# Performance work log

Hardware: AMD Instinct MI355X
Metric: run time of the kernel (lower is better)

Reference implementation:

```python
import jax, jax.numpy as jnp
import numpy as np


def setup_inputs() -> dict:
    key = jax.random.key(0)
    k1, k2, k3 = jax.random.split(key, 3)
    B, Lc, Lq, D = 16, 1024, 1024, 256
    context_features = jax.random.normal(k1, (B, Lc, D), dtype=jnp.float32)
    question_features = jax.random.normal(k2, (B, Lq, D), dtype=jnp.float32)
    # nn.Linear(3D, 1, bias=False) weight, stored transposed as [3D, 1]
    weight = jax.random.normal(k3, (3 * D, 1), dtype=jnp.float32) * (1.0 / np.sqrt(3 * D))
    return {"context_features": context_features, "question_features": question_features, "weight": weight}


def reference(context_features, question_features, weight):
    # Trilinear similarity: sim[b,i,j] = [c_i ; q_j ; c_i*q_j] @ w
    # Decompose w = [wc ; wq ; wm] (each D) to avoid the O(B*Lc*Lq*3D) tensor:
    # sim = c@wc + q@wq + (c*wm) @ q^T   -- exact same math as the concat+Linear.
    D = context_features.shape[-1]
    w = weight[:, 0]
    wc, wq, wm = w[:D], w[D:2 * D], w[2 * D:]
    sim = (
        jnp.einsum('bcd,d->bc', context_features, wc)[:, :, None]
        + jnp.einsum('bqd,d->bq', question_features, wq)[:, None, :]
        + jnp.einsum('bcd,bqd->bcq', context_features * wm, question_features)
    )  # [B, Lc, Lq]
    weight_c2q = jax.nn.softmax(sim, axis=-1)                      # [B, Lc, Lq]
    c2q = jnp.einsum('bcq,bqd->bcd', weight_c2q, question_features)
    weight_q2c = jax.nn.softmax(jnp.max(sim, axis=2), axis=-1)     # [B, Lc]
    q2c = jnp.einsum('bc,bcd->bd', weight_q2c, context_features)   # [B, D]
    q2c = jnp.broadcast_to(q2c[:, None, :], c2q.shape)             # repeat over Lc
    return (c2q, q2c)
```

## Files before the change

### kernel.cpp

```cpp
#include <hip/hip_runtime.h>
#include <math.h>

#define BB 16
#define LC 1024
#define LQ 1024
#define DD 256

#define CTB 64
#define QTB 64
#define QT_S 72

typedef __attribute__((ext_vector_type(4))) float f32x4;
typedef __attribute__((ext_vector_type(8))) short bf16x8;
typedef __attribute__((ext_vector_type(4))) short bf16x4;

__device__ inline short f2bf(float f) {
    union { float f; unsigned u; } v; v.f = f;
    unsigned r = v.u + 0x7FFFu + ((v.u >> 16) & 1u);
    return (short)(r >> 16);
}


__global__ __launch_bounds__(256) void k_prep(const float* __restrict__ qst,
                                              const float* __restrict__ w,
                                              short* __restrict__ Qbf,
                                              short* __restrict__ Qtbf,
                                              float* __restrict__ qterm) {
    __shared__ short Qt_lds[DD][QT_S];
    int t = threadIdx.x;
    int qt = blockIdx.x;
    int b  = blockIdx.y;
    int wv4 = t >> 6;
    int l   = t & 63;
    int lx  = l & 15;
    int ls  = l >> 4;

    #pragma unroll
    for (int kq = 0; kq < 4; ++kq) {
        int ql = 16 * wv4 + 4 * kq + ls;
        float qpart = 0.f;
        #pragma unroll
        for (int jd = 0; jd < 4; ++jd) {
            int d0 = 64 * jd + 4 * lx;
            float4 x = *(const float4*)(qst + ((size_t)(b * LQ + qt * QTB + ql)) * DD + d0);
            float4 wq = *(const float4*)(w + DD + d0);
            qpart += x.x * wq.x + x.y * wq.y + x.z * wq.z + x.w * wq.w;
            bf16x4 o;
            o[0] = f2bf(x.x); o[1] = f2bf(x.y); o[2] = f2bf(x.z); o[3] = f2bf(x.w);
            *(bf16x4*)(Qbf + ((size_t)(b * LQ + qt * QTB + ql)) * DD + d0) = o;
            float X[4] = {x.x, x.y, x.z, x.w};
            float P1[4], X1[4], P2[4], X2[4];
            #pragma unroll
            for (int e = 0; e < 4; ++e) P1[e] = __shfl_xor(X[e ^ 1], 16);
            #pragma unroll
            for (int e = 0; e < 4; ++e) X1[e] = ((ls & 1) == (e & 1)) ? X[e] : P1[e];
            #pragma unroll
            for (int e = 0; e < 4; ++e) P2[e] = __shfl_xor(X1[e ^ 2], 32);
            #pragma unroll
            for (int e = 0; e < 4; ++e) X2[e] = ((ls & 2) == (e & 2)) ? X1[e] : P2[e];
            int dl = 64 * jd + 4 * lx + ls;
            bf16x4 ot;
            ot[0] = f2bf(X2[0]); ot[1] = f2bf(X2[1]); ot[2] = f2bf(X2[2]); ot[3] = f2bf(X2[3]);
            *(bf16x4*)&Qt_lds[dl][16 * wv4 + 4 * kq] = ot;
        }
        qpart += __shfl_xor(qpart, 1);
        qpart += __shfl_xor(qpart, 2);
        qpart += __shfl_xor(qpart, 4);
        qpart += __shfl_xor(qpart, 8);
        if (lx == 0) qterm[b * LQ + qt * QTB + ql] = qpart;
    }
    __syncthreads();
    #pragma unroll
    for (int rep = 0; rep < 8; ++rep) {
        int d   = rep * 32 + (t >> 3);
        int qch = t & 7;
        bf16x8 v = *(const bf16x8*)&Qt_lds[d][8 * qch];
        *(bf16x8*)(Qtbf + ((size_t)(b * DD + d)) * LQ + qt * QTB + 8 * qch) = v;
    }
}

__global__ __launch_bounds__(512) void k_main(const float* __restrict__ ctx,
                                              const short* __restrict__ Qbf,
                                              const short* __restrict__ Qtbf,
                                              const float* __restrict__ wght,
                                              const float* __restrict__ ws,
                                              float* __restrict__ out,
                                              float* __restrict__ rowmax_out) {
    __shared__ short CMp[4 * 8 * 512];
    __shared__ short sPp[2][4 * 2 * 512];
    __shared__ float scaleS[2][CTB];
    __shared__ float mS[2][CTB], lS[2][CTB];
    __shared__ float ctermS[2][CTB];
    __shared__ float mergebuf[4 * 64 * 20];

    const int t  = threadIdx.x;
    const int wv = t >> 6;
    const int g  = wv >> 2;
    const int w4 = wv & 3;
    const int l  = t & 63;
    const int lx = l & 15;
    const int ls = l >> 4;
    const int bid = blockIdx.x;
    const int b  = bid & 15;
    const int c0 = (bid >> 4) * CTB;

    const float* qterm = ws;

    {
        const int kh = g * 4;
        int cl = 16 * w4 + lx;
        float cpart = 0.f;
        #pragma unroll
        for (int kq = 0; kq < 4; ++kq) {
            int kk = kh + kq;
            int d0 = 32 * kk + 8 * ls;
            const float4 x0 = *(const float4*)(ctx + ((size_t)(b * LC + c0 + cl)) * DD + d0);
            const float4 x1 = *(const float4*)(ctx + ((size_t)(b * LC + c0 + cl)) * DD + d0 + 4);
            const float4 w0 = *(const float4*)(wght + 2 * DD + d0);
            const float4 w1 = *(const float4*)(wght + 2 * DD + d0 + 4);
            const float4 c0v = *(const float4*)(wght + d0);
            const float4 c1v = *(const float4*)(wght + d0 + 4);
            cpart += x0.x * c0v.x + x0.y * c0v.y + x0.z * c0v.z + x0.w * c0v.w
                   + x1.x * c1v.x + x1.y * c1v.y + x1.z * c1v.z + x1.w * c1v.w;
            bf16x8 o;
            o[0] = f2bf(x0.x * w0.x); o[1] = f2bf(x0.y * w0.y);
            o[2] = f2bf(x0.z * w0.z); o[3] = f2bf(x0.w * w0.w);
            o[4] = f2bf(x1.x * w1.x); o[5] = f2bf(x1.y * w1.y);
            o[6] = f2bf(x1.z * w1.z); o[7] = f2bf(x1.w * w1.w);
            *(bf16x8*)&CMp[(w4 * 8 + kk) * 512 + l * 8] = o;
        }
        cpart += __shfl_xor(cpart, 16);
        cpart += __shfl_xor(cpart, 32);
        if (ls == 0) ctermS[g][cl] = cpart;
    }

    float mrun[4], lrun[4];
    f32x4 oacc[4][4];
    #pragma unroll
    for (int r = 0; r < 4; ++r) { mrun[r] = -1e30f; lrun[r] = 0.f; }
    #pragma unroll
    for (int cf = 0; cf < 4; ++cf)
        #pragma unroll
        for (int df = 0; df < 4; ++df)
            oacc[cf][df] = (f32x4){0.f, 0.f, 0.f, 0.f};

    __syncthreads();

    for (int it = 0; it < 8; ++it) {
        const int qtile = 2 * it + g;
        const size_t qbase = (size_t)b * LQ + qtile * QTB;

        f32x4 sacc[4];
        #pragma unroll
        for (int f = 0; f < 4; ++f) sacc[f] = (f32x4){0.f, 0.f, 0.f, 0.f};
        bf16x8 bA[4][4], bB[4][4];
        #pragma unroll
        for (int kk = 0; kk < 4; ++kk)
            #pragma unroll
            for (int f = 0; f < 4; ++f)
                bA[kk][f] = *(const bf16x8*)(Qbf + (qbase + 16 * f + lx) * DD + 32 * kk + 8 * ls);
        bf16x8 acur = *(const bf16x8*)&CMp[(w4 * 8 + 0) * 512 + l * 8];
        #pragma unroll
        for (int kk = 0; kk < 4; ++kk) {
            bf16x8 anext = *(const bf16x8*)&CMp[(w4 * 8 + kk + 1) * 512 + l * 8];
            #pragma unroll
            for (int f = 0; f < 4; ++f)
                bB[kk][f] = *(const bf16x8*)(Qbf + (qbase + 16 * f + lx) * DD + 32 * (kk + 4) + 8 * ls);
            #pragma unroll
            for (int f = 0; f < 4; ++f)
                sacc[f] = __builtin_amdgcn_mfma_f32_16x16x32_bf16(acur, bA[kk][f], sacc[f], 0, 0, 0);
            acur = anext;
        }
        #pragma unroll
        for (int kk = 4; kk < 8; ++kk) {
            bf16x8 anext = (kk < 7) ? *(const bf16x8*)&CMp[(w4 * 8 + kk + 1) * 512 + l * 8] : acur;
            #pragma unroll
            for (int f = 0; f < 4; ++f)
                sacc[f] = __builtin_amdgcn_mfma_f32_16x16x32_bf16(acur, bB[kk - 4][f], sacc[f], 0, 0, 0);
            acur = anext;
        }

        bf16x8 qtb[2][4];
        #pragma unroll
        for (int kk = 0; kk < 2; ++kk)
            #pragma unroll
            for (int df = 0; df < 4; ++df)
                qtb[kk][df] = *(const bf16x8*)(Qtbf + ((size_t)(b * DD + 64 * w4 + 16 * df + lx)) * LQ
                                               + qtile * QTB + 32 * kk + 8 * ls);

        float qv[4];
        #pragma unroll
        for (int f = 0; f < 4; ++f) qv[f] = qterm[qbase + 16 * f + lx];
        #pragma unroll
        for (int f = 0; f < 4; ++f) {
            #pragma unroll
            for (int r = 0; r < 4; ++r) sacc[f][r] += qv[f];
        }
        float scl[4];
        #pragma unroll
        for (int r = 0; r < 4; ++r) {
            float v = fmaxf(fmaxf(sacc[0][r], sacc[1][r]), fmaxf(sacc[2][r], sacc[3][r]));
            v = fmaxf(v, __shfl_xor(v, 1));
            v = fmaxf(v, __shfl_xor(v, 2));
            v = fmaxf(v, __shfl_xor(v, 4));
            v = fmaxf(v, __shfl_xor(v, 8));
            float mn = fmaxf(mrun[r], v);
            scl[r] = __expf(mrun[r] - mn);
            mrun[r] = mn;
            lrun[r] *= scl[r];
        }
        float p[4][4];
        float rs[4] = {0.f, 0.f, 0.f, 0.f};
        #pragma unroll
        for (int f = 0; f < 4; ++f)
            #pragma unroll
            for (int r = 0; r < 4; ++r) {
                p[f][r] = __expf(sacc[f][r] - mrun[r]);
                rs[r] += p[f][r];
            }
        #pragma unroll
        for (int r = 0; r < 4; ++r) {
            float v = rs[r];
            v += __shfl_xor(v, 1);
            v += __shfl_xor(v, 2);
            v += __shfl_xor(v, 4);
            v += __shfl_xor(v, 8);
            lrun[r] += v;
        }
        #pragma unroll
        for (int f = 0; f < 4; ++f) {
            #pragma unroll
            for (int r = 0; r < 4; ++r) {
                int cl = 16 * w4 + 4 * ls + r;
                int ql = 16 * f + lx;
                int idx = ((cl >> 4) * 2 + (ql >> 5)) * 512 + ((cl & 15) + 16 * ((ql >> 3) & 3)) * 8 + (ql & 7);
                sPp[g][idx] = f2bf(p[f][r]);
            }
        }
        if (lx == 0) {
            #pragma unroll
            for (int r = 0; r < 4; ++r) scaleS[g][16 * w4 + 4 * ls + r] = scl[r];
        }
        __syncthreads();

        #pragma unroll
        for (int cf = 0; cf < 4; ++cf) {
            #pragma unroll
            for (int r = 0; r < 4; ++r) {
                float s = scaleS[g][16 * cf + 4 * ls + r];
                #pragma unroll
                for (int df = 0; df < 4; ++df) oacc[cf][df][r] *= s;
            }
        }
        bf16x8 pa[2][4];
        #pragma unroll
        for (int kk = 0; kk < 2; ++kk)
            #pragma unroll
            for (int cf = 0; cf < 4; ++cf)
                pa[kk][cf] = *(const bf16x8*)&sPp[g][(cf * 2 + kk) * 512 + l * 8];
        #pragma unroll
        for (int kk = 0; kk < 2; ++kk)
            #pragma unroll
            for (int df = 0; df < 4; ++df)
                #pragma unroll
                for (int cf = 0; cf < 4; ++cf)
                    oacc[cf][df] = __builtin_amdgcn_mfma_f32_16x16x32_bf16(pa[kk][cf], qtb[kk][df], oacc[cf][df], 0, 0, 0);
        __syncthreads();
    }

    if (lx == 0) {
        #pragma unroll
        for (int r = 0; r < 4; ++r) {
            mS[g][16 * w4 + 4 * ls + r] = mrun[r];
            lS[g][16 * w4 + 4 * ls + r] = lrun[r];
        }
    }
    __syncthreads();

    float alpha[4][4], ltot[4][4], mtot[4][4];
    #pragma unroll
    for (int cf = 0; cf < 4; ++cf) {
        #pragma unroll
        for (int r = 0; r < 4; ++r) {
            int cl = 16 * cf + 4 * ls + r;
            float m0 = mS[0][cl], m1 = mS[1][cl];
            float mx = fmaxf(m0, m1);
            float a0 = __expf(m0 - mx), a1 = __expf(m1 - mx);
            mtot[cf][r] = mx;
            ltot[cf][r] = a0 * lS[0][cl] + a1 * lS[1][cl];
            alpha[cf][r] = (g == 0) ? a0 : a1;
        }
    }
    #pragma unroll
    for (int cf = 0; cf < 4; ++cf) {
        #pragma unroll
        for (int df = 0; df < 4; ++df)
            #pragma unroll
            for (int r = 0; r < 4; ++r)
                oacc[cf][df][r] *= alpha[cf][r];
    }
    #pragma unroll
    for (int cf = 0; cf < 4; ++cf) {
        if (g == 1) {
            #pragma unroll
            for (int df = 0; df < 4; ++df)
                *(f32x4*)&mergebuf[(w4 * 64 + l) * 20 + df * 4] = oacc[cf][df];
        }
        __syncthreads();
        if (g == 0) {
            #pragma unroll
            for (int df = 0; df < 4; ++df) {
                f32x4 v = *(const f32x4*)&mergebuf[(w4 * 64 + l) * 20 + df * 4];
                oacc[cf][df][0] += v[0]; oacc[cf][df][1] += v[1];
                oacc[cf][df][2] += v[2]; oacc[cf][df][3] += v[3];
            }
        }
        __syncthreads();
    }

    if (g == 0) {
        if (wv == 0 && lx == 0) {
            #pragma unroll
            for (int cf = 0; cf < 4; ++cf)
                #pragma unroll
                for (int r = 0; r < 4; ++r) {
                    int cl = 16 * cf + 4 * ls + r;
                    int c = b * LC + c0 + cl;
                    rowmax_out[c] = mtot[cf][r] + ctermS[0][cl] + ctermS[1][cl];
                }
        }
        #pragma unroll
        for (int cf = 0; cf < 4; ++cf) {
            #pragma unroll
            for (int r = 0; r < 4; ++r) {
                float inv = 1.0f / ltot[cf][r];
                size_t row = (size_t)(b * LC + c0 + 16 * cf + 4 * ls + r) * DD;
                #pragma unroll
                for (int df = 0; df < 4; ++df)
                    out[row + 64 * w4 + 16 * df + lx] = oacc[cf][df][r] * inv;
            }
        }
    }
}

__global__ __launch_bounds__(256) void k_q2c(const float* __restrict__ ctx,
                                             const float* __restrict__ rowmax,
                                             float* __restrict__ q2cvec) {
    __shared__ float sm[LC];
    __shared__ float red[256];
    int b = blockIdx.x;
    int chunk = blockIdx.y;
    int t = threadIdx.x;
    const float* rm = rowmax + b * LC;

    float lmax = -1e30f;
    #pragma unroll
    for (int k = 0; k < 4; ++k) {
        float v = rm[t + k * 256];
        sm[t + k * 256] = v;
        lmax = fmaxf(lmax, v);
    }
    red[t] = lmax;
    __syncthreads();
    for (int s = 128; s > 0; s >>= 1) {
        if (t < s) red[t] = fmaxf(red[t], red[t + s]);
        __syncthreads();
    }
    float gmax = red[0];
    __syncthreads();
    float lsum = 0.f;
    #pragma unroll
    for (int k = 0; k < 4; ++k) {
        int i = t + k * 256;
        float e = __expf(sm[i] - gmax);
        sm[i] = e;
        lsum += e;
    }
    red[t] = lsum;
    __syncthreads();
    for (int s = 128; s > 0; s >>= 1) {
        if (t < s) red[t] += red[t + s];
        __syncthreads();
    }
    float inv = 1.0f / red[0];

    int c0 = chunk * 32;
    float acc = 0.f;
    for (int c = c0; c < c0 + 32; ++c)
        acc += sm[c] * ctx[(size_t)(b * LC + c) * DD + t];
    atomicAdd(&q2cvec[b * DD + t], acc * inv);
}

__global__ __launch_bounds__(256) void k_bcast(const float* __restrict__ q2cvec,
                                               float* __restrict__ out2) {
    int g = blockIdx.x * 256 + threadIdx.x;
    int b  = g >> 16;
    int d4 = g & 63;
    ((float4*)out2)[g] = ((const float4*)q2cvec)[b * 64 + d4];
}

extern "C" void kernel_launch(void* const* d_in, const int* in_sizes, int n_in,
                              void* d_out, int out_size, void* d_ws, size_t ws_size,
                              hipStream_t stream) {
    const float* ctx = (const float*)d_in[0];
    const float* qst = (const float*)d_in[1];
    const float* w   = (const float*)d_in[2];
    float* out  = (float*)d_out;
    float* out2 = out + (size_t)BB * LC * DD;
    float* ws   = (float*)d_ws;

    float* qterm  = ws;
    float* rowmax = ws + 32768;
    float* q2cvec = ws + 49152;
    short* Qbf  = (short*)out2;
    short* Qtbf = Qbf + (size_t)BB * LQ * DD;

    hipMemsetAsync(q2cvec, 0, BB * DD * sizeof(float), stream);

    k_prep<<<dim3(LQ / QTB, BB), 256, 0, stream>>>(qst, w, Qbf, Qtbf, qterm);

    k_main<<<(LC / CTB) * BB, 512, 0, stream>>>(ctx, Qbf, Qtbf, w, ws, out, rowmax);

    k_q2c<<<dim3(BB, 32), 256, 0, stream>>>(ctx, rowmax, q2cvec);

    k_bcast<<<(BB * LC * DD / 4) / 256, 256, 0, stream>>>(q2cvec, out2);
}
```

Measured before the change: 185.9 us.

## Split query loop across four wave groups with 1024-thread blocks; fold memset into prep

The main kernel now runs 1024 threads per block, so four wave groups each handle a quarter of the query tiles instead of two groups handling half each. Their flash-style partial softmax states are then merged through a shared LDS pool that is reused for the P tiles and the merge buffer. The separate memset of the q2c accumulator is moved into the prep kernel to save a launch. This gives more parallelism per context tile and fewer serial iterations per wave. In exchange it adds three sequential merge rounds with barriers, and the larger register and LDS footprint per block may reduce occupancy.

```diff
diff --git a/kernel.cpp b/kernel.cpp
--- a/kernel.cpp
+++ b/kernel.cpp
@@ -25,7 +25,8 @@
                                               const float* __restrict__ w,
                                               short* __restrict__ Qbf,
                                               short* __restrict__ Qtbf,
-                                              float* __restrict__ qterm) {
+                                              float* __restrict__ qterm,
+                                              float* __restrict__ q2cvec) {
     __shared__ short Qt_lds[DD][QT_S];
     int t = threadIdx.x;
     int qt = blockIdx.x;
@@ -34,6 +35,8 @@
     int l   = t & 63;
     int lx  = l & 15;
     int ls  = l >> 4;
+
+    if (qt == 0) q2cvec[b * DD + t] = 0.f;
 
     #pragma unroll
     for (int kq = 0; kq < 4; ++kq) {
@@ -79,19 +82,20 @@
     }
 }
 
-__global__ __launch_bounds__(512) void k_main(const float* __restrict__ ctx,
-                                              const short* __restrict__ Qbf,
-                                              const short* __restrict__ Qtbf,
-                                              const float* __restrict__ wght,
-                                              const float* __restrict__ ws,
-                                              float* __restrict__ out,
-                                              float* __restrict__ rowmax_out) {
-    __shared__ short CMp[4 * 8 * 512];
-    __shared__ short sPp[2][4 * 2 * 512];
-    __shared__ float scaleS[2][CTB];
-    __shared__ float mS[2][CTB], lS[2][CTB];
+__global__ __launch_bounds__(1024) void k_main(const float* __restrict__ ctx,
+                                               const short* __restrict__ Qbf,
+                                               const short* __restrict__ Qtbf,
+                                               const float* __restrict__ wght,
+                                               const float* __restrict__ ws,
+                                               float* __restrict__ out,
+                                               float* __restrict__ rowmax_out) {
+    __shared__ __align__(16) char pool[32768 + 256 * 68 * 4];
+    short* CMp = (short*)pool;
+    short* sPp = (short*)(pool + 32768);
+    float* mergebuf = (float*)(pool + 32768);
+    __shared__ float scaleS[4][CTB];
+    __shared__ float mS[4][CTB], lS[4][CTB];
     __shared__ float ctermS[2][CTB];
-    __shared__ float mergebuf[4 * 64 * 20];
 
     const int t  = threadIdx.x;
     const int wv = t >> 6;
@@ -106,7 +110,7 @@
 
     const float* qterm = ws;
 
-    {
+    if (g < 2) {
         const int kh = g * 4;
         int cl = 16 * w4 + lx;
         float cpart = 0.f;
@@ -146,8 +150,8 @@
 
     __syncthreads();
 
-    for (int it = 0; it < 8; ++it) {
-        const int qtile = 2 * it + g;
+    for (int it = 0; it < 4; ++it) {
+        const int qtile = 4 * it + g;
         const size_t qbase = (size_t)b * LQ + qtile * QTB;
 
         f32x4 sacc[4];
@@ -234,7 +238,7 @@
                 int cl = 16 * w4 + 4 * ls + r;
                 int ql = 16 * f + lx;
                 int idx = ((cl >> 4) * 2 + (ql >> 5)) * 512 + ((cl & 15) + 16 * ((ql >> 3) & 3)) * 8 + (ql & 7);
-                sPp[g][idx] = f2bf(p[f][r]);
+                sPp[g * 4096 + idx] = f2bf(p[f][r]);
             }
         }
         if (lx == 0) {
@@ -257,7 +261,7 @@
         for (int kk = 0; kk < 2; ++kk)
             #pragma unroll
             for (int cf = 0; cf < 4; ++cf)
-                pa[kk][cf] = *(const bf16x8*)&sPp[g][(cf * 2 + kk) * 512 + l * 8];
+                pa[kk][cf] = *(const bf16x8*)&sPp[g * 4096 + (cf * 2 + kk) * 512 + l * 8];
         #pragma unroll
         for (int kk = 0; kk < 2; ++kk)
             #pragma unroll
@@ -283,37 +287,42 @@
         #pragma unroll
         for (int r = 0; r < 4; ++r) {
             int cl = 16 * cf + 4 * ls + r;
-            float m0 = mS[0][cl], m1 = mS[1][cl];
-            float mx = fmaxf(m0, m1);
-            float a0 = __expf(m0 - mx), a1 = __expf(m1 - mx);
+            float mx = fmaxf(fmaxf(mS[0][cl], mS[1][cl]), fmaxf(mS[2][cl], mS[3][cl]));
+            float lt = 0.f;
+            #pragma unroll
+            for (int j = 0; j < 4; ++j) lt += __expf(mS[j][cl] - mx) * lS[j][cl];
             mtot[cf][r] = mx;
-            ltot[cf][r] = a0 * lS[0][cl] + a1 * lS[1][cl];
-            alpha[cf][r] = (g == 0) ? a0 : a1;
-        }
-    }
-    #pragma unroll
-    for (int cf = 0; cf < 4; ++cf) {
+            ltot[cf][r] = lt;
+            alpha[cf][r] = __expf(mS[g][cl] - mx);
+        }
+    }
+    #pragma unroll
+    for (int cf = 0; cf < 4; ++cf)
         #pragma unroll
         for (int df = 0; df < 4; ++df)
             #pragma unroll
             for (int r = 0; r < 4; ++r)
                 oacc[cf][df][r] *= alpha[cf][r];
-    }
-    #pragma unroll
-    for (int cf = 0; cf < 4; ++cf) {
-        if (g == 1) {
-            #pragma unroll
-            for (int df = 0; df < 4; ++df)
-                *(f32x4*)&mergebuf[(w4 * 64 + l) * 20 + df * 4] = oacc[cf][df];
+
+    const int slot = (w4 * 64 + l) * 68;
+    for (int src = 1; src < 4; ++src) {
+        if (g == src) {
+            #pragma unroll
+            for (int cf = 0; cf < 4; ++cf)
+                #pragma unroll
+                for (int df = 0; df < 4; ++df)
+                    *(f32x4*)&mergebuf[slot + (cf * 4 + df) * 4] = oacc[cf][df];
         }
         __syncthreads();
         if (g == 0) {
             #pragma unroll
-            for (int df = 0; df < 4; ++df) {
-                f32x4 v = *(const f32x4*)&mergebuf[(w4 * 64 + l) * 20 + df * 4];
-                oacc[cf][df][0] += v[0]; oacc[cf][df][1] += v[1];
-                oacc[cf][df][2] += v[2]; oacc[cf][df][3] += v[3];
-            }
+            for (int cf = 0; cf < 4; ++cf)
+                #pragma unroll
+                for (int df = 0; df < 4; ++df) {
+                    f32x4 v = *(const f32x4*)&mergebuf[slot + (cf * 4 + df) * 4];
+                    oacc[cf][df][0] += v[0]; oacc[cf][df][1] += v[1];
+                    oacc[cf][df][2] += v[2]; oacc[cf][df][3] += v[3];
+                }
         }
         __syncthreads();
     }
@@ -415,11 +424,9 @@
     short* Qbf  = (short*)out2;
     short* Qtbf = Qbf + (size_t)BB * LQ * DD;
 
-    hipMemsetAsync(q2cvec, 0, BB * DD * sizeof(float), stream);
-
-    k_prep<<<dim3(LQ / QTB, BB), 256, 0, stream>>>(qst, w, Qbf, Qtbf, qterm);
-
-    k_main<<<(LC / CTB) * BB, 512, 0, stream>>>(ctx, Qbf, Qtbf, w, ws, out, rowmax);
+    k_prep<<<dim3(LQ / QTB, BB), 256, 0, stream>>>(qst, w, Qbf, Qtbf, qterm, q2cvec);
+
+    k_main<<<(LC / CTB) * BB, 1024, 0, stream>>>(ctx, Qbf, Qtbf, w, ws, out, rowmax);
 
     k_q2c<<<dim3(BB, 32), 256, 0, stream>>>(ctx, rowmax, q2cvec);
 
```

After: 263.5 us. 1.42x slower.
